# Kernel tuning notes

Hardware: AMD Instinct MI355X
Metric: run time of the kernel (lower is better)

Reference implementation:

```python
import jax, jax.numpy as jnp
import numpy as np

N, E, F, D, C, L, H = 50000, 800000, 256, 128, 40, 5, 8
HD = D // H
EPS = 1e-5


def setup_inputs() -> dict:
    key = jax.random.key(0)
    keys = iter(jax.random.split(key, 40))
    def w(shape, fan_in):
        return jax.random.normal(next(keys), shape, jnp.float32) / np.sqrt(fan_in)
    return dict(
        x=jax.random.normal(next(keys), (N, F), jnp.float32),
        edge_src=jax.random.randint(next(keys), (E,), 0, N, jnp.int32),
        edge_dst=jax.random.randint(next(keys), (E,), 0, N, jnp.int32),
        Wi=w((F, D), F), bi=jnp.zeros((D,), jnp.float32),
        Wq=w((L, D, D), D), bq=jnp.zeros((L, D), jnp.float32),
        Wk=w((L, D, D), D), bk=jnp.zeros((L, D), jnp.float32),
        Wv=w((L, D, D), D), bv=jnp.zeros((L, D), jnp.float32),
        Wo=w((L, D, D), D), bo=jnp.zeros((L, D), jnp.float32),
        g1=jnp.ones((L, D), jnp.float32), b1=jnp.zeros((L, D), jnp.float32),
        Wf1=w((L, D, 2 * D), D), bf1=jnp.zeros((L, 2 * D), jnp.float32),
        Wf2=w((L, 2 * D, D), 2 * D), bf2=jnp.zeros((L, D), jnp.float32),
        g_out=jnp.ones((D,), jnp.float32), b_out=jnp.zeros((D,), jnp.float32),
        Wout=w((D, C), D), bout=jnp.zeros((C,), jnp.float32),
    )


def _ln(x, g, b):
    mu = x.mean(-1, keepdims=True)
    var = ((x - mu) ** 2).mean(-1, keepdims=True)
    return (x - mu) / jnp.sqrt(var + EPS) * g + b


def _attn(h, src, dst, Wq, bq, Wk, bk, Wv, bv, Wo, bo):
    n = h.shape[0]
    q = (h @ Wq + bq).reshape(n, H, HD)
    k = (h @ Wk + bk).reshape(n, H, HD)
    v = (h @ Wv + bv).reshape(n, H, HD)
    # u_dot_v: per-edge dot(q[src], k[dst]) per head -> [E, H]
    scores = jnp.einsum('ehd,ehd->eh', q[src], k[dst]) / np.sqrt(HD).astype(np.float32)
    # edge_softmax over incoming edges of each destination node
    m = jax.ops.segment_max(scores, dst, num_segments=n)
    ex = jnp.exp(scores - m[dst])
    denom = jax.ops.segment_sum(ex, dst, num_segments=n)
    p = ex / denom[dst]
    # u_mul_e_sum: sum_e v[src] * p  scattered to dst
    agg = jax.ops.segment_sum(v[src] * p[:, :, None], dst, num_segments=n)
    return agg.reshape(n, D) @ Wo + bo


def reference(x, edge_src, edge_dst, Wi, bi, Wq, bq, Wk, bk, Wv, bv, Wo, bo,
              g1, b1, Wf1, bf1, Wf2, bf2, g_out, b_out, Wout, bout):
    h = jax.nn.relu(x @ Wi + bi)
    for i in range(L):
        r = _ln(h, g1[i], b1[i])
        r = _attn(r, edge_src, edge_dst, Wq[i], bq[i], Wk[i], bk[i], Wv[i], bv[i], Wo[i], bo[i])
        h = h + r
        # NOTE: original module reuses norms_1 here (norms_2 unused) - reproduced
        r = _ln(h, g1[i], b1[i])
        r = jax.nn.relu(r @ Wf1[i] + bf1[i]) @ Wf2[i] + bf2[i]
        h = h + r
    mid = h
    out = _ln(h, g_out, b_out) @ Wout + bout  # squeeze(1) is a no-op (nclass != 1)
    return (mid, out)
```

## Files before the change

### kernel.cpp

```cpp
#include <hip/hip_runtime.h>
#include <hip/hip_bf16.h>

typedef __hip_bfloat16 bf16;
typedef __attribute__((ext_vector_type(8))) short bf16x8;
typedef __attribute__((ext_vector_type(4))) float f32x4;

#define N_NODES 50000
#define N_EDGES 800000
#define DIM 128
#define QKVW 384

__device__ __forceinline__ void storeO(float* p, float v){ *p = v; }
__device__ __forceinline__ void storeO(bf16* p, float v){ *p = __float2bfloat16(v); }
__device__ __forceinline__ float bfu2f(unsigned short u){
  return __uint_as_float(((unsigned)u) << 16);
}
__device__ __forceinline__ unsigned short f2bfbits(float f){
  bf16 t = __float2bfloat16(f);
  return *reinterpret_cast<unsigned short*>(&t);
}

__global__ void fill_kernel(unsigned* __restrict__ p, unsigned val, int n){
  int i = blockIdx.x * blockDim.x + threadIdx.x;
  if (i < n) p[i] = val;
}

__global__ void prep_w_kernel(const float* __restrict__ W, bf16* __restrict__ Wt,
    int K, int M, int L){
  int idx = blockIdx.x * blockDim.x + threadIdx.x;
  int tot = L * K * M;
  if (idx >= tot) return;
  int l = idx / (K * M), r = idx - l * (K * M);
  int m = r / K, k = r - m * K;
  Wt[idx] = __float2bfloat16(W[(size_t)l * K * M + (size_t)k * M + m]);
}

__global__ void prep_qkvw_kernel(const float* __restrict__ Wq, const float* __restrict__ Wk,
    const float* __restrict__ Wv, bf16* __restrict__ Wt){
  int idx = blockIdx.x * blockDim.x + threadIdx.x;
  if (idx >= 5 * QKVW * 128) return;
  int l = idx / (QKVW * 128), r = idx - l * (QKVW * 128);
  int m = r / 128, k = r - m * 128;
  const float* src = (m < 128) ? (Wq + (size_t)l * 16384 + (size_t)k * 128 + m)
                   : (m < 256) ? (Wk + (size_t)l * 16384 + (size_t)k * 128 + (m - 128))
                               : (Wv + (size_t)l * 16384 + (size_t)k * 128 + (m - 256));
  Wt[idx] = __float2bfloat16(*src);
}

__global__ void pack_qkvbias_kernel(const float* __restrict__ bq, const float* __restrict__ bk,
    const float* __restrict__ bv, float* __restrict__ bqkv){
  int i = blockIdx.x * blockDim.x + threadIdx.x;
  if (i >= 5 * QKVW) return;
  int l = i / QKVW, j = i - l * QKVW;
  float v = (j < 128) ? bq[l * 128 + j] : (j < 256) ? bk[l * 128 + j - 128] : bv[l * 128 + j - 256];
  bqkv[i] = v;
}

__global__ void hist_kernel(const int* __restrict__ dst, int* __restrict__ counts, int E){
  int e = blockIdx.x * blockDim.x + threadIdx.x;
  if (e < E) atomicAdd(counts + dst[e], 1);
}

__global__ __launch_bounds__(256) void blockscan_kernel(const int* __restrict__ counts,
    int* __restrict__ rowptr, int* __restrict__ bsum, int n){
  __shared__ int buf[256];
  int t = threadIdx.x, i = blockIdx.x * 256 + t;
  int x = (i < n) ? counts[i] : 0;
  buf[t] = x; __syncthreads();
  #pragma unroll
  for (int off = 1; off < 256; off <<= 1){
    int v = (t >= off) ? buf[t - off] : 0;
    __syncthreads(); buf[t] += v; __syncthreads();
  }
  if (i < n) rowptr[i] = buf[t] - x;
  if (t == 255) bsum[blockIdx.x] = buf[255];
}

__global__ __launch_bounds__(256) void scanb_kernel(int* __restrict__ bsum, int nb){
  __shared__ int buf[256];
  int t = threadIdx.x;
  int x = (t < nb) ? bsum[t] : 0;
  buf[t] = x; __syncthreads();
  #pragma unroll
  for (int off = 1; off < 256; off <<= 1){
    int v = (t >= off) ? buf[t - off] : 0;
    __syncthreads(); buf[t] += v; __syncthreads();
  }
  if (t < nb) bsum[t] = buf[t] - x;
  if (t == nb - 1) bsum[nb] = buf[t];
}

__global__ void addoff_kernel(int* __restrict__ rowptr, const int* __restrict__ bsum,
    int n, int nb){
  int i = blockIdx.x * blockDim.x + threadIdx.x;
  if (i < n) rowptr[i] += bsum[i >> 8];
  if (i == 0) rowptr[n] = bsum[nb];
}

__global__ void scatter_kernel(const int* __restrict__ src, const int* __restrict__ dst,
    const int* __restrict__ rowptr, int* __restrict__ cursor,
    int* __restrict__ srclist, int E){
  int e = blockIdx.x * blockDim.x + threadIdx.x;
  if (e >= E) return;
  int d = dst[e];
  int pos = rowptr[d] + atomicAdd(cursor + d, 1);
  srclist[pos] = src[e];
}

__global__ __launch_bounds__(256) void attn_kernel(
    const int* __restrict__ rowptr, const int* __restrict__ srclist,
    const bf16* __restrict__ qkv, bf16* __restrict__ agg, int n){
  int d = blockIdx.x * 4 + (threadIdx.x >> 6);
  int lane = threadIdx.x & 63;
  if (d >= n) return;
  const ushort2* kp = (const ushort2*)(qkv + (size_t)d * QKVW + 128);
  ushort2 ku = kp[lane];
  float k0 = bfu2f(ku.x) * 0.25f, k1 = bfu2f(ku.y) * 0.25f;
  float den = 0.f, acc0 = 0.f, acc1 = 0.f;
  int e = rowptr[d], e1 = rowptr[d + 1];
  for (; e + 8 <= e1; e += 8){
    int s[8];
    #pragma unroll
    for (int j = 0; j < 8; j++) s[j] = srclist[e + j];
    ushort2 qu[8], vu[8];
    #pragma unroll
    for (int j = 0; j < 8; j++) qu[j] = ((const ushort2*)(qkv + (size_t)s[j] * QKVW))[lane];
    #pragma unroll
    for (int j = 0; j < 8; j++) vu[j] = ((const ushort2*)(qkv + (size_t)s[j] * QKVW + 256))[lane];
    float p[8];
    #pragma unroll
    for (int j = 0; j < 8; j++) p[j] = fmaf(bfu2f(qu[j].x), k0, bfu2f(qu[j].y) * k1);
    #pragma unroll
    for (int j = 0; j < 8; j++){
      p[j] += __shfl_xor(p[j], 1);
      p[j] += __shfl_xor(p[j], 2);
      p[j] += __shfl_xor(p[j], 4);
    }
    #pragma unroll
    for (int j = 0; j < 8; j++){
      float w = __expf(p[j]);
      acc0 = fmaf(w, bfu2f(vu[j].x), acc0);
      acc1 = fmaf(w, bfu2f(vu[j].y), acc1);
      den += w;
    }
  }
  for (; e < e1; e++){
    int s = srclist[e];
    ushort2 qu = ((const ushort2*)(qkv + (size_t)s * QKVW))[lane];
    ushort2 vu = ((const ushort2*)(qkv + (size_t)s * QKVW + 256))[lane];
    float p = fmaf(bfu2f(qu.x), k0, bfu2f(qu.y) * k1);
    p += __shfl_xor(p, 1); p += __shfl_xor(p, 2); p += __shfl_xor(p, 4);
    float w = __expf(p);
    acc0 = fmaf(w, bfu2f(vu.x), acc0);
    acc1 = fmaf(w, bfu2f(vu.y), acc1);
    den += w;
  }
  float inv = (den > 0.f) ? 1.f / den : 0.f;
  bf16* ap = agg + (size_t)d * DIM + lane * 2;
  ap[0] = __float2bfloat16(acc0 * inv);
  ap[1] = __float2bfloat16(acc1 * inv);
}

template<int KT, int MT, typename AT, bool FUSELN, bool RELU, bool RESID, typename OT>
__global__ __launch_bounds__(256, (KT == 128) ? 4 : 2) void pgemm4(
    const AT* __restrict__ A, const float* __restrict__ lng, const float* __restrict__ lnb,
    const bf16* __restrict__ Wt, const float* __restrict__ bias,
    const float* __restrict__ resid, OT* __restrict__ out, float* __restrict__ out2,
    int n, int M){
  constexpr int CPR = KT / 8;
  constexpr int CPT = (64 * CPR) / 256;
  constexpr int NMT = MT / 64;
  constexpr int NKS = KT / 32;
  __shared__ short Ash[64][KT + 8];
  int tid = threadIdx.x;
  int wv = tid >> 6, lane = tid & 63;
  int l15 = lane & 15, quad = lane >> 4;
  int bm = blockIdx.x * 64;

  bf16x8 wf[2][NKS];
  auto loadW = [&](int mt, int b){
    int col = mt * 64 + wv * 16 + l15;
    #pragma unroll
    for (int ks = 0; ks < NKS; ks++){
      int4 w = make_int4(0, 0, 0, 0);
      if (col < M) w = *(const int4*)(Wt + (size_t)col * KT + ks * 32 + quad * 8);
      wf[b][ks] = *(bf16x8*)&w;
    }
  };
  loadW(0, 0);

  #pragma unroll
  for (int i = 0; i < CPT; i++){
    int c = tid + i * 256;
    int row = c / CPR, off = (c - row * CPR) * 8;
    int gr = bm + row;
    if constexpr (sizeof(AT) == 4){
      float va[8];
      if (gr < n){
        float4 f0 = *(const float4*)(A + (size_t)gr * KT + off);
        float4 f1 = *(const float4*)(A + (size_t)gr * KT + off + 4);
        va[0]=f0.x; va[1]=f0.y; va[2]=f0.z; va[3]=f0.w;
        va[4]=f1.x; va[5]=f1.y; va[6]=f1.z; va[7]=f1.w;
      } else {
        #pragma unroll
        for (int j = 0; j < 8; j++) va[j] = 0.f;
      }
      if constexpr (FUSELN){
        float s = va[0]+va[1]+va[2]+va[3]+va[4]+va[5]+va[6]+va[7];
        s += __shfl_xor(s, 1); s += __shfl_xor(s, 2);
        s += __shfl_xor(s, 4); s += __shfl_xor(s, 8);
        float mu = s * (1.f / 128.f);
        float vs = 0.f;
        #pragma unroll
        for (int j = 0; j < 8; j++){ float dd = va[j] - mu; vs += dd * dd; }
        vs += __shfl_xor(vs, 1); vs += __shfl_xor(vs, 2);
        vs += __shfl_xor(vs, 4); vs += __shfl_xor(vs, 8);
        float rs = rsqrtf(vs * (1.f / 128.f) + 1e-5f);
        float4 g0 = *(const float4*)(lng + off);
        float4 g1 = *(const float4*)(lng + off + 4);
        float4 b0 = *(const float4*)(lnb + off);
        float4 b1 = *(const float4*)(lnb + off + 4);
        va[0]=(va[0]-mu)*rs*g0.x+b0.x; va[1]=(va[1]-mu)*rs*g0.y+b0.y;
        va[2]=(va[2]-mu)*rs*g0.z+b0.z; va[3]=(va[3]-mu)*rs*g0.w+b0.w;
        va[4]=(va[4]-mu)*rs*g1.x+b1.x; va[5]=(va[5]-mu)*rs*g1.y+b1.y;
        va[6]=(va[6]-mu)*rs*g1.z+b1.z; va[7]=(va[7]-mu)*rs*g1.w+b1.w;
      }
      unsigned short tmp[8];
      #pragma unroll
      for (int j = 0; j < 8; j++) tmp[j] = f2bfbits(va[j]);
      *(int4*)(&Ash[row][off]) = *(const int4*)tmp;
    } else {
      int4 av = make_int4(0, 0, 0, 0);
      if (gr < n) av = *(const int4*)(A + (size_t)gr * KT + off);
      *(int4*)(&Ash[row][off]) = av;
    }
  }
  __syncthreads();

  #pragma unroll
  for (int mt = 0; mt < NMT; mt++){
    int b = mt & 1;
    if (mt + 1 < NMT) loadW(mt + 1, b ^ 1);
    f32x4 acc[4];
    #pragma unroll
    for (int i = 0; i < 4; i++) acc[i] = (f32x4){0.f, 0.f, 0.f, 0.f};
    #pragma unroll
    for (int ks = 0; ks < NKS; ks++){
      bf16x8 bfrag = wf[b][ks];
      #pragma unroll
      for (int mi = 0; mi < 4; mi++){
        bf16x8 afrag = *(const bf16x8*)(&Ash[mi * 16 + l15][ks * 32 + quad * 8]);
        acc[mi] = __builtin_amdgcn_mfma_f32_16x16x32_bf16(afrag, bfrag, acc[mi], 0, 0, 0);
      }
    }
    int col = mt * 64 + wv * 16 + l15;
    if (col < M){
      float bval = bias[col];
      #pragma unroll
      for (int mi = 0; mi < 4; mi++){
        int row0 = bm + mi * 16 + quad * 4;
        #pragma unroll
        for (int rg = 0; rg < 4; rg++){
          int grow = row0 + rg;
          if (grow >= n) continue;
          float v = acc[mi][rg] + bval;
          if (RELU) v = fmaxf(v, 0.f);
          if (RESID) v += resid[(size_t)grow * M + col];
          storeO(out + (size_t)grow * M + col, v);
          if (out2) out2[(size_t)grow * M + col] = v;
        }
      }
    }
  }
}

extern "C" void kernel_launch(void* const* d_in, const int* in_sizes, int n_in,
                              void* d_out, int out_size, void* d_ws, size_t ws_size,
                              hipStream_t stream) {
  const float* x    = (const float*)d_in[0];
  const int*  esrc  = (const int*)d_in[1];
  const int*  edst  = (const int*)d_in[2];
  const float* Wi   = (const float*)d_in[3];
  const float* bi   = (const float*)d_in[4];
  const float* Wq   = (const float*)d_in[5];
  const float* bq   = (const float*)d_in[6];
  const float* Wk   = (const float*)d_in[7];
  const float* bk   = (const float*)d_in[8];
  const float* Wv   = (const float*)d_in[9];
  const float* bv   = (const float*)d_in[10];
  const float* Wo   = (const float*)d_in[11];
  const float* bo   = (const float*)d_in[12];
  const float* g1   = (const float*)d_in[13];
  const float* b1   = (const float*)d_in[14];
  const float* Wf1  = (const float*)d_in[15];
  const float* bf1  = (const float*)d_in[16];
  const float* Wf2  = (const float*)d_in[17];
  const float* bf2  = (const float*)d_in[18];
  const float* gout = (const float*)d_in[19];
  const float* bout_ln = (const float*)d_in[20];
  const float* Wout = (const float*)d_in[21];
  const float* bout = (const float*)d_in[22];

  const size_t ND = (size_t)N_NODES * DIM;
  float* ws = (float*)d_ws;
  float* h   = ws;
  bf16* agg  = (bf16*)(ws + ND);
  bf16* qkv  = (bf16*)(ws + ND + ND / 2);
  bf16* mid  = qkv;
  float* after_qkv = ws + ND + ND / 2 + ((size_t)N_NODES * QKVW) / 2;
  bf16* Wit    = (bf16*)after_qkv;
  bf16* Wqkvt  = Wit + 128 * 256;
  bf16* Wot    = Wqkvt + 5 * QKVW * 128;
  bf16* Wf1t   = Wot + 5 * 128 * 128;
  bf16* Wf2t   = Wf1t + 5 * 256 * 128;
  bf16* Woutt  = Wf2t + 5 * 128 * 256;
  float* bqkv  = (float*)(Woutt + 40 * 128);
  int* rowptr  = (int*)(bqkv + 5 * QKVW);
  int* cnt     = rowptr + N_NODES + 1;
  int* bsum    = cnt + N_NODES;
  int* srclist = bsum + 200;

  dim3 B(256);
  const int EB = (N_EDGES + 255) / 256;
  const int NB = (N_NODES + 255) / 256;
  const int NSB = (N_NODES + 255) / 256;
  dim3 Grow(782);

  prep_w_kernel<<<(1 * 256 * 128 + 255) / 256, B, 0, stream>>>(Wi, Wit, 256, 128, 1);
  prep_qkvw_kernel<<<(5 * QKVW * 128 + 255) / 256, B, 0, stream>>>(Wq, Wk, Wv, Wqkvt);
  prep_w_kernel<<<(5 * 128 * 128 + 255) / 256, B, 0, stream>>>(Wo, Wot, 128, 128, 5);
  prep_w_kernel<<<(5 * 128 * 256 + 255) / 256, B, 0, stream>>>(Wf1, Wf1t, 128, 256, 5);
  prep_w_kernel<<<(5 * 256 * 128 + 255) / 256, B, 0, stream>>>(Wf2, Wf2t, 256, 128, 5);
  prep_w_kernel<<<(1 * 128 * 40 + 255) / 256, B, 0, stream>>>(Wout, Woutt, 128, 40, 1);
  pack_qkvbias_kernel<<<(5 * QKVW + 255) / 256, B, 0, stream>>>(bq, bk, bv, bqkv);
  fill_kernel<<<NB, B, 0, stream>>>((unsigned*)cnt, 0u, N_NODES);
  hist_kernel<<<EB, B, 0, stream>>>(edst, cnt, N_EDGES);
  blockscan_kernel<<<NSB, B, 0, stream>>>(cnt, rowptr, bsum, N_NODES);
  scanb_kernel<<<1, B, 0, stream>>>(bsum, NSB);
  addoff_kernel<<<NB, B, 0, stream>>>(rowptr, bsum, N_NODES, NSB);
  fill_kernel<<<NB, B, 0, stream>>>((unsigned*)cnt, 0u, N_NODES);
  scatter_kernel<<<EB, B, 0, stream>>>(esrc, edst, rowptr, cnt, srclist, N_EDGES);

  pgemm4<256, 128, float, false, true, false, float><<<Grow, B, 0, stream>>>(
      x, nullptr, nullptr, Wit, bi, nullptr, h, nullptr, N_NODES, 128);

  for (int l = 0; l < 5; l++){
    pgemm4<128, 384, float, true, false, false, bf16><<<Grow, B, 0, stream>>>(
        h, g1 + l * DIM, b1 + l * DIM, Wqkvt + (size_t)l * QKVW * 128,
        bqkv + l * QKVW, nullptr, qkv, nullptr, N_NODES, QKVW);
    attn_kernel<<<12500, B, 0, stream>>>(rowptr, srclist, qkv, agg, N_NODES);
    pgemm4<128, 128, bf16, false, false, true, float><<<Grow, B, 0, stream>>>(
        agg, nullptr, nullptr, Wot + (size_t)l * 128 * 128, bo + l * DIM,
        h, h, nullptr, N_NODES, 128);
    pgemm4<128, 256, float, true, true, false, bf16><<<Grow, B, 0, stream>>>(
        h, g1 + l * DIM, b1 + l * DIM, Wf1t + (size_t)l * 256 * 128,
        bf1 + l * 2 * DIM, nullptr, mid, nullptr, N_NODES, 256);
    float* out2 = (l == 4) ? (float*)d_out : nullptr;
    pgemm4<256, 128, bf16, false, false, true, float><<<Grow, B, 0, stream>>>(
        mid, nullptr, nullptr, Wf2t + (size_t)l * 128 * 256, bf2 + l * DIM,
        h, h, out2, N_NODES, 128);
  }

  pgemm4<128, 64, float, true, false, false, float><<<Grow, B, 0, stream>>>(
      h, gout, bout_ln, Woutt, bout, nullptr, ((float*)d_out) + ND, nullptr, N_NODES, 40);
}
```

Measured before the change: 1.083 ms.

## Reorder QKV packing to Q,V,K and process four edges per wavefront in attention

The packed QKV weights and biases are reordered so Q and V sit next to each other, which lets each edge's Q and V be read with nearby 16-byte loads. The attention kernel now splits each 64-lane wavefront into four 16-lane groups. Each group handles a different edge and each lane holds 8 dims, which is half a head, so the head dot product needs only one shuffle. Partial softmax sums and accumulators are merged across groups with cross-lane shuffles at the end. This widens memory accesses and raises edge-level parallelism, at the cost of wasted work in the masked tail iterations and extra reduction shuffles.

```diff
diff --git a/kernel.cpp b/kernel.cpp
--- a/kernel.cpp
+++ b/kernel.cpp
@@ -42,8 +42,8 @@
   int l = idx / (QKVW * 128), r = idx - l * (QKVW * 128);
   int m = r / 128, k = r - m * 128;
   const float* src = (m < 128) ? (Wq + (size_t)l * 16384 + (size_t)k * 128 + m)
-                   : (m < 256) ? (Wk + (size_t)l * 16384 + (size_t)k * 128 + (m - 128))
-                               : (Wv + (size_t)l * 16384 + (size_t)k * 128 + (m - 256));
+                   : (m < 256) ? (Wv + (size_t)l * 16384 + (size_t)k * 128 + (m - 128))
+                               : (Wk + (size_t)l * 16384 + (size_t)k * 128 + (m - 256));
   Wt[idx] = __float2bfloat16(*src);
 }
 
@@ -52,7 +52,7 @@
   int i = blockIdx.x * blockDim.x + threadIdx.x;
   if (i >= 5 * QKVW) return;
   int l = i / QKVW, j = i - l * QKVW;
-  float v = (j < 128) ? bq[l * 128 + j] : (j < 256) ? bk[l * 128 + j - 128] : bv[l * 128 + j - 256];
+  float v = (j < 128) ? bq[l * 128 + j] : (j < 256) ? bv[l * 128 + j - 128] : bk[l * 128 + j - 256];
   bqkv[i] = v;
 }
 
@@ -113,52 +113,72 @@
   int d = blockIdx.x * 4 + (threadIdx.x >> 6);
   int lane = threadIdx.x & 63;
   if (d >= n) return;
-  const ushort2* kp = (const ushort2*)(qkv + (size_t)d * QKVW + 128);
-  ushort2 ku = kp[lane];
-  float k0 = bfu2f(ku.x) * 0.25f, k1 = bfu2f(ku.y) * 0.25f;
-  float den = 0.f, acc0 = 0.f, acc1 = 0.f;
+  int eslot = lane >> 4;
+  int t = lane & 15;
+  float kf[8];
+  {
+    const int4* kp = (const int4*)(qkv + (size_t)d * QKVW + 256 + t * 8);
+    int4 kv = kp[0];
+    const unsigned* ku = (const unsigned*)&kv;
+    #pragma unroll
+    for (int j = 0; j < 4; j++){
+      kf[2*j]   = __uint_as_float(ku[j] << 16) * 0.25f;
+      kf[2*j+1] = __uint_as_float(ku[j] & 0xffff0000u) * 0.25f;
+    }
+  }
+  float acc[8];
+  #pragma unroll
+  for (int j = 0; j < 8; j++) acc[j] = 0.f;
+  float den = 0.f;
   int e = rowptr[d], e1 = rowptr[d + 1];
-  for (; e + 8 <= e1; e += 8){
-    int s[8];
-    #pragma unroll
-    for (int j = 0; j < 8; j++) s[j] = srclist[e + j];
-    ushort2 qu[8], vu[8];
-    #pragma unroll
-    for (int j = 0; j < 8; j++) qu[j] = ((const ushort2*)(qkv + (size_t)s[j] * QKVW))[lane];
-    #pragma unroll
-    for (int j = 0; j < 8; j++) vu[j] = ((const ushort2*)(qkv + (size_t)s[j] * QKVW + 256))[lane];
-    float p[8];
-    #pragma unroll
-    for (int j = 0; j < 8; j++) p[j] = fmaf(bfu2f(qu[j].x), k0, bfu2f(qu[j].y) * k1);
-    #pragma unroll
-    for (int j = 0; j < 8; j++){
-      p[j] += __shfl_xor(p[j], 1);
-      p[j] += __shfl_xor(p[j], 2);
-      p[j] += __shfl_xor(p[j], 4);
-    }
-    #pragma unroll
-    for (int j = 0; j < 8; j++){
-      float w = __expf(p[j]);
-      acc0 = fmaf(w, bfu2f(vu[j].x), acc0);
-      acc1 = fmaf(w, bfu2f(vu[j].y), acc1);
-      den += w;
-    }
-  }
-  for (; e < e1; e++){
-    int s = srclist[e];
-    ushort2 qu = ((const ushort2*)(qkv + (size_t)s * QKVW))[lane];
-    ushort2 vu = ((const ushort2*)(qkv + (size_t)s * QKVW + 256))[lane];
-    float p = fmaf(bfu2f(qu.x), k0, bfu2f(qu.y) * k1);
-    p += __shfl_xor(p, 1); p += __shfl_xor(p, 2); p += __shfl_xor(p, 4);
-    float w = __expf(p);
-    acc0 = fmaf(w, bfu2f(vu.x), acc0);
-    acc1 = fmaf(w, bfu2f(vu.y), acc1);
-    den += w;
-  }
-  float inv = (den > 0.f) ? 1.f / den : 0.f;
-  bf16* ap = agg + (size_t)d * DIM + lane * 2;
-  ap[0] = __float2bfloat16(acc0 * inv);
-  ap[1] = __float2bfloat16(acc1 * inv);
+  for (; e < e1; e += 8){
+    int eeA = e + eslot, eeB = e + 4 + eslot;
+    int sA = srclist[(eeA < e1) ? eeA : (e1 - 1)];
+    int sB = srclist[(eeB < e1) ? eeB : (e1 - 1)];
+    const int4* qpA = (const int4*)(qkv + (size_t)sA * QKVW + t * 8);
+    const int4* qpB = (const int4*)(qkv + (size_t)sB * QKVW + t * 8);
+    int4 qA = qpA[0];
+    int4 vA = qpA[16];
+    int4 qB = qpB[0];
+    int4 vB = qpB[16];
+    float pA = 0.f, pB = 0.f;
+    const unsigned* qa = (const unsigned*)&qA;
+    const unsigned* qb = (const unsigned*)&qB;
+    #pragma unroll
+    for (int j = 0; j < 4; j++){
+      pA = fmaf(__uint_as_float(qa[j] << 16),          kf[2*j],   pA);
+      pA = fmaf(__uint_as_float(qa[j] & 0xffff0000u),  kf[2*j+1], pA);
+      pB = fmaf(__uint_as_float(qb[j] << 16),          kf[2*j],   pB);
+      pB = fmaf(__uint_as_float(qb[j] & 0xffff0000u),  kf[2*j+1], pB);
+    }
+    pA += __shfl_xor(pA, 1);
+    pB += __shfl_xor(pB, 1);
+    float wA = (eeA < e1) ? __expf(pA) : 0.f;
+    float wB = (eeB < e1) ? __expf(pB) : 0.f;
+    den += wA + wB;
+    const unsigned* va = (const unsigned*)&vA;
+    const unsigned* vb = (const unsigned*)&vB;
+    #pragma unroll
+    for (int j = 0; j < 4; j++){
+      acc[2*j]   = fmaf(wA, __uint_as_float(va[j] << 16),         acc[2*j]);
+      acc[2*j+1] = fmaf(wA, __uint_as_float(va[j] & 0xffff0000u), acc[2*j+1]);
+      acc[2*j]   = fmaf(wB, __uint_as_float(vb[j] << 16),         acc[2*j]);
+      acc[2*j+1] = fmaf(wB, __uint_as_float(vb[j] & 0xffff0000u), acc[2*j+1]);
+    }
+  }
+  #pragma unroll
+  for (int m = 16; m <= 32; m <<= 1){
+    den += __shfl_xor(den, m);
+    #pragma unroll
+    for (int j = 0; j < 8; j++) acc[j] += __shfl_xor(acc[j], m);
+  }
+  if (eslot == 0){
+    float inv = (den > 0.f) ? 1.f / den : 0.f;
+    unsigned short o[8];
+    #pragma unroll
+    for (int j = 0; j < 8; j++) o[j] = f2bfbits(acc[j] * inv);
+    *(int4*)(agg + (size_t)d * DIM + t * 8) = *(const int4*)o;
+  }
 }
 
 template<int KT, int MT, typename AT, bool FUSELN, bool RELU, bool RESID, typename OT>
```

New measurement: 1.060 ms. -2.1%, faster.
